# Kernel tuning notes

Measured on AMD Instinct MI355X. Metric: run time of the kernel, lower is better.

Reference implementation:

```python
import jax, jax.numpy as jnp
import numpy as np
from jax import lax

B, T = 64, 256
V, E, H, O = 50000, 256, 512, 50

def _xavier(key, shape):
    fan_in, fan_out = shape[1], shape[0]
    std = float(np.sqrt(2.0 / (fan_in + fan_out)))
    return jax.random.normal(key, shape, dtype=jnp.float32) * std

def lstm_scan(x, W_ih, W_hh, b, h0, c0):
    # x: (B, T, Din); precompute input projection for all timesteps
    xg = jnp.einsum('btd,gd->btg', x, W_ih) + b  # (B, T, 4H)
    def step(carry, xg_t):
        h, c = carry
        g = xg_t + h @ W_hh.T
        i, f, gg, o = jnp.split(g, 4, axis=-1)
        i = jax.nn.sigmoid(i); f = jax.nn.sigmoid(f)
        gg = jnp.tanh(gg); o = jax.nn.sigmoid(o)
        c = f * c + i * gg
        h = o * jnp.tanh(c)
        return (h, c), h
    _, hs = lax.scan(step, (h0, c0), jnp.transpose(xg, (1, 0, 2)))
    return jnp.transpose(hs, (1, 0, 2))  # (B, T, H)

def bilstm(x, W_ih, W_hh, b, h0, c0):
    # Faithful to source bugs: output_backward == output_forward flipped on BATCH dim
    out_f = lstm_scan(x, W_ih, W_hh, b, h0, c0)
    return jnp.concatenate([out_f, out_f[::-1]], axis=-1)  # (B, T, 2H)

def setup_inputs() -> dict:
    key = jax.random.key(0)
    ks = jax.random.split(key, 14)
    x = jax.random.randint(ks[0], (B, T), 0, V + 1, dtype=jnp.int32)
    emb = jax.random.normal(ks[1], (V + 1, E), dtype=jnp.float32)
    emb = emb.at[0].set(0.0)  # padding_idx=0
    s = 1.0 / np.sqrt(H)
    W_ih1 = jax.random.uniform(ks[2], (4 * H, E), minval=-s, maxval=s, dtype=jnp.float32)
    W_hh1 = jax.random.uniform(ks[3], (4 * H, H), minval=-s, maxval=s, dtype=jnp.float32)
    b1 = jax.random.uniform(ks[4], (4 * H,), minval=-s, maxval=s, dtype=jnp.float32)
    W_ih2 = jax.random.uniform(ks[5], (4 * H, 2 * H), minval=-s, maxval=s, dtype=jnp.float32)
    W_hh2 = jax.random.uniform(ks[6], (4 * H, H), minval=-s, maxval=s, dtype=jnp.float32)
    b2 = jax.random.uniform(ks[7], (4 * H,), minval=-s, maxval=s, dtype=jnp.float32)
    h01 = _xavier(ks[8], (B, H)); c01 = _xavier(ks[9], (B, H))
    h02 = _xavier(ks[10], (B, H)); c02 = _xavier(ks[11], (B, H))
    Wfc = jax.random.normal(ks[12], (O, 2 * H), dtype=jnp.float32) * 0.02
    bfc = jnp.zeros((O,), dtype=jnp.float32)
    return {"x": x, "emb": emb, "W_ih1": W_ih1, "W_hh1": W_hh1, "b1": b1,
            "h01": h01, "c01": c01, "W_ih2": W_ih2, "W_hh2": W_hh2, "b2": b2,
            "h02": h02, "c02": c02, "Wfc": Wfc, "bfc": bfc}

def reference(x, emb, W_ih1, W_hh1, b1, h01, c01, W_ih2, W_hh2, b2, h02, c02, Wfc, bfc):
    out = emb[x]                                   # (B, T, E) embedding lookup
    out = bilstm(out, W_ih1, W_hh1, b1, h01, c01)  # (B, T, 2H)
    out = bilstm(out, W_ih2, W_hh2, b2, h02, c02)  # (B, T, 2H)
    # dropout is identity at inference
    logits = jnp.einsum('btd,od->bto', out, Wfc) + bfc
    return jax.nn.log_softmax(logits, axis=-1)
```

## Files before the change

kernel.cpp:

```cpp
#include <hip/hip_runtime.h>


#define B_ 64
#define T_ 256
#define E_ 256
#define H_ 512
#define G_ 2048
#define O_ 50
#define NROW (B_ * T_)
#define RING 16

typedef unsigned short u16;
typedef unsigned int u32;
typedef unsigned long long u64;
typedef short bf16x8 __attribute__((ext_vector_type(8)));
typedef u16 u16x4 __attribute__((ext_vector_type(4)));
typedef u32 u32x4 __attribute__((ext_vector_type(4)));
typedef float f32x4 __attribute__((ext_vector_type(4)));

#define LD_AG(p)    __hip_atomic_load((p), __ATOMIC_RELAXED, __HIP_MEMORY_SCOPE_AGENT)
#define ST_AG(p, v) __hip_atomic_store((p), (v), __ATOMIC_RELAXED, __HIP_MEMORY_SCOPE_AGENT)

__device__ __forceinline__ u16 f2bf(float f) {
    unsigned u = __float_as_uint(f);
    return (u16)((u + 0x7fffu + ((u >> 16) & 1u)) >> 16);
}
__device__ __forceinline__ float bf2f(u16 x) {
    return __uint_as_float(((u32)x) << 16);
}
__device__ __forceinline__ float sigm(float x) {
    x = fminf(fmaxf(x, -30.f), 30.f);
    return 1.f / (1.f + __expf(-x));
}
__device__ __forceinline__ float tanh_f(float x) {
    x = fminf(fmaxf(x, -15.f), 15.f);
    float e = __expf(2.f * x);
    return (e - 1.f) / (e + 1.f);
}
__device__ __forceinline__ bf16x8 pack8(const float* p) {
    float4 v0 = *(const float4*)p;
    float4 v1 = *(const float4*)(p + 4);
    bf16x8 bb;
    bb[0] = (short)f2bf(v0.x); bb[1] = (short)f2bf(v0.y);
    bb[2] = (short)f2bf(v0.z); bb[3] = (short)f2bf(v0.w);
    bb[4] = (short)f2bf(v1.x); bb[5] = (short)f2bf(v1.y);
    bb[6] = (short)f2bf(v1.z); bb[7] = (short)f2bf(v1.w);
    return bb;
}

__global__ __launch_bounds__(256) void wfc_pad(
    const float* __restrict__ Wfc, u16* __restrict__ outp)
{
    int i = blockIdx.x * 256 + threadIdx.x;
    int row = i >> 8, c4 = (i & 255) * 4;
    u16x4 o = { 0, 0, 0, 0 };
    if (row < O_) {
        float4 v = *(const float4*)&Wfc[(size_t)row * 1024 + c4];
        o = u16x4{ f2bf(v.x), f2bf(v.y), f2bf(v.z), f2bf(v.w) };
    }
    *(u16x4*)&outp[(size_t)row * 1024 + c4] = o;
}

__global__ __launch_bounds__(256) void gemm_fused(
    const int* __restrict__ x, const float* __restrict__ emb,
    const float* __restrict__ Wih1, const float* __restrict__ b1,
    u16* __restrict__ C)
{
    __shared__ u16 Asm[128][40];
    __shared__ u16 Bsm[128][40];
    const int tid = threadIdx.x, lane = tid & 63, wave = tid >> 6;
    const int wr = wave >> 1, wc = wave & 1;
    const int bm = blockIdx.y, bn = blockIdx.x;
    f32x4 acc[4][4] = {};
    const int r = tid >> 1, kc = (tid & 1) * 16;
    const int grow = bm * 128 + r;
    const int xi = x[grow];
    const float* ag = emb  + (size_t)xi * E_;
    const float* bg = Wih1 + (size_t)(bn * 128 + r) * E_;
    for (int k0 = 0; k0 < E_; k0 += 32) {
        int col = k0 + kc;
        __syncthreads();
        *(bf16x8*)&Asm[r][kc]     = pack8(ag + col);
        *(bf16x8*)&Asm[r][kc + 8] = pack8(ag + col + 8);
        *(bf16x8*)&Bsm[r][kc]     = pack8(bg + col);
        *(bf16x8*)&Bsm[r][kc + 8] = pack8(bg + col + 8);
        __syncthreads();
        bf16x8 af[4], bf[4];
        #pragma unroll
        for (int mt = 0; mt < 4; mt++)
            af[mt] = *(const bf16x8*)&Asm[wr * 64 + mt * 16 + (lane & 15)][(lane >> 4) * 8];
        #pragma unroll
        for (int nt = 0; nt < 4; nt++)
            bf[nt] = *(const bf16x8*)&Bsm[wc * 64 + nt * 16 + (lane & 15)][(lane >> 4) * 8];
        #pragma unroll
        for (int mt = 0; mt < 4; mt++)
            #pragma unroll
            for (int nt = 0; nt < 4; nt++)
                acc[mt][nt] = __builtin_amdgcn_mfma_f32_16x16x32_bf16(
                    af[mt], bf[nt], acc[mt][nt], 0, 0, 0);
    }
    #pragma unroll
    for (int mt = 0; mt < 4; mt++) {
        #pragma unroll
        for (int nt = 0; nt < 4; nt++) {
            int col = bn * 128 + wc * 64 + nt * 16 + (lane & 15);
            float bv = b1[col];
            #pragma unroll
            for (int rr = 0; rr < 4; rr++) {
                int row = bm * 128 + wr * 64 + mt * 16 + (lane >> 4) * 4 + rr;
                C[(size_t)row * G_ + col] = f2bf(acc[mt][nt][rr] + bv);
            }
        }
    }
}

__global__ __launch_bounds__(512, 2) void scan12(
    const u16* __restrict__ xgb,
    const float* __restrict__ Whh1,
    const float* __restrict__ h01, const float* __restrict__ c01,
    u32* h1pub,
    u32* hx1,
    const float* __restrict__ Wih2,
    const float* __restrict__ Whh2,
    const float* __restrict__ b2,
    const float* __restrict__ h02, const float* __restrict__ c02,
    u32* ring,
    u32* hx2,
    u32* h2pk,
    int* sents)
{
    __shared__ u16 hl[16][520];
    __shared__ u16 a1cat[16][1032];
    __shared__ float glds[4][8][68];
    const int tid = threadIdx.x, lane = tid & 63, wave = tid >> 6;
    const int idx = blockIdx.x;
    const u64 tmask = 0xffff0000ffff0000ull;
    int budget = 1 << 20;

    if (idx < 64) {
        const int grp = idx & 7, ug = idx >> 3;
        const int gw = wave >> 1, uh = wave & 1;
        for (int j = tid; j < 8 * 260; j += 512) {
            int rw = 8 + j / 260, cl = (j % 260) * 2;
            *(u32*)&hl[rw][cl] = 0;
        }
        bf16x8 breg0[16], breg1[16];
        #pragma unroll
        for (int tt = 0; tt < 2; tt++) {
            const float* wr0 = Whh1
                + (size_t)(gw * H_ + ug * 64 + uh * 32 + tt * 16 + (lane & 15)) * H_
                + ((lane >> 4) * 8);
            #pragma unroll
            for (int kk = 0; kk < 16; kk++) {
                bf16x8 bb = pack8(wr0 + kk * 32);
                if (tt == 0) breg0[kk] = bb; else breg1[kk] = bb;
            }
        }
        const int bb_ = tid >> 6, uu = tid & 63;
        const int brow = grp * 8 + bb_, ucol = ug * 64 + uu;
        float c = c01[brow * H_ + ucol];
        #pragma unroll
        for (int j = 0; j < 8; ++j) {
            int k = tid + j * 512;
            int prow = k >> 9, pcol = k & 511;
            ST_AG(hx1 + (size_t)(grp * 8 + prow) * H_ + pcol,
                  (1u << 16) | (u32)f2bf(h01[(grp * 8 + prow) * H_ + pcol]));
        }
        const int crow = tid >> 6, ccol = (tid & 63) * 8;
        int* mysent = sents + grp * 32 + ug;
        __syncthreads();

        #pragma unroll 1
        for (int t = 0; t < T_; ++t) {
            const size_t xb = ((size_t)brow * T_ + t) * G_ + ucol;
            u16 xi = xgb[xb], xf = xgb[xb + 512];
            u16 xgg = xgb[xb + 1024], xo = xgb[xb + 1536];

            u64* src = (u64*)(hx1 + (size_t)(t & 1) * (B_ * H_)
                              + (size_t)(grp * 8 + crow) * H_ + ccol);
            const u32 wt = (u32)(t + 1);
            const u64 want = ((u64)wt << 16) | ((u64)wt << 48);
            u64 v0 = LD_AG(src + 0), v1 = LD_AG(src + 1);
            u64 v2 = LD_AG(src + 2), v3 = LD_AG(src + 3);
            int spin = 0;
            while ((((v0 ^ want) | (v1 ^ want) | (v2 ^ want) | (v3 ^ want)) & tmask) != 0) {
                if (--budget < 0) break;
                if (++spin > 2) __builtin_amdgcn_s_sleep(1);
                if ((v0 ^ want) & tmask) v0 = LD_AG(src + 0);
                if ((v1 ^ want) & tmask) v1 = LD_AG(src + 1);
                if ((v2 ^ want) & tmask) v2 = LD_AG(src + 2);
                if ((v3 ^ want) & tmask) v3 = LD_AG(src + 3);
            }
            u32x4 pk = { (u32)(v0 & 0xffff) | ((u32)(v0 >> 32) << 16),
                         (u32)(v1 & 0xffff) | ((u32)(v1 >> 32) << 16),
                         (u32)(v2 & 0xffff) | ((u32)(v2 >> 32) << 16),
                         (u32)(v3 & 0xffff) | ((u32)(v3 >> 32) << 16) };
            *(u32x4*)&hl[crow][ccol] = pk;
            __syncthreads();

            f32x4 a0 = {0,0,0,0}, a1 = {0,0,0,0}, a2 = {0,0,0,0}, a3 = {0,0,0,0};
            const int ar = lane & 15, ac = (lane >> 4) * 8;
            #pragma unroll
            for (int kk = 0; kk < 16; kk += 2) {
                bf16x8 f0 = *(const bf16x8*)&hl[ar][ac + kk * 32];
                bf16x8 f1 = *(const bf16x8*)&hl[ar][ac + (kk + 1) * 32];
                a0 = __builtin_amdgcn_mfma_f32_16x16x32_bf16(f0, breg0[kk],     a0, 0, 0, 0);
                a1 = __builtin_amdgcn_mfma_f32_16x16x32_bf16(f1, breg0[kk + 1], a1, 0, 0, 0);
                a2 = __builtin_amdgcn_mfma_f32_16x16x32_bf16(f0, breg1[kk],     a2, 0, 0, 0);
                a3 = __builtin_amdgcn_mfma_f32_16x16x32_bf16(f1, breg1[kk + 1], a3, 0, 0, 0);
            }
            #pragma unroll
            for (int rr = 0; rr < 4; rr++) {
                int br = (lane >> 4) * 4 + rr;
                if (br < 8) {
                    glds[gw][br][uh * 32 + (lane & 15)]      = a0[rr] + a1[rr];
                    glds[gw][br][uh * 32 + 16 + (lane & 15)] = a2[rr] + a3[rr];
                }
            }
            __syncthreads();

            float ip = glds[0][bb_][uu] + bf2f(xi);
            float fp = glds[1][bb_][uu] + bf2f(xf);
            float gp = glds[2][bb_][uu] + bf2f(xgg);
            float op = glds[3][bb_][uu] + bf2f(xo);
            float gi = sigm(ip), gf = sigm(fp), gc = tanh_f(gp), go = sigm(op);
            c = gf * c + gi * gc;
            float h = go * tanh_f(c);
            u32 me = f2bf(h);
            ST_AG(hx1 + (size_t)((t + 1) & 1) * (B_ * H_) + (size_t)brow * H_ + ucol,
                  ((u32)(t + 2) << 16) | me);
            u32 ot = (u32)__shfl_xor((int)me, 1);
            if (!(uu & 1))
                ST_AG(h1pub + ((size_t)brow * T_ + t) * 256 + (ucol >> 1),
                      me | (ot << 16));
            if (tid == 0) ST_AG(mysent, t + 1);
        }
        __syncthreads();
        if (tid == 0) ST_AG(mysent, T_ + 1);

    } else if (idx < 192) {
        const int bg = idx & 7, gg = (idx - 64) >> 3;
        for (int j = tid; j < 8 * 516; j += 512) {
            int rw = 8 + j / 516, cl = (j % 516) * 2;
            *(u32*)&a1cat[rw][cl] = 0;
        }
        const int gcol = gg * 128 + wave * 16 + (lane & 15);
        bf16x8 bi[32];
        {
            const float* wr0 = Wih2 + (size_t)gcol * 1024 + ((lane >> 4) * 8);
            #pragma unroll
            for (int kk = 0; kk < 32; kk++) bi[kk] = pack8(wr0 + kk * 32);
        }
        const float bias = b2[gcol];
        const int crow = tid >> 6, ccol = (tid & 63) * 16;
        const int myb  = bg * 8 + crow;
        const int myfb = (7 - bg) * 8 + (7 - crow);
        const u32* __restrict__ hbase =
            h1pub + (size_t)((ccol < 512) ? myb : myfb) * T_ * 256;
        const int  cadj  = (ccol < 512) ? (ccol >> 1) : ((ccol - 512) >> 1);
        __syncthreads();

        #pragma unroll 1
        for (int t = 0; t < T_; ++t) {
            if (tid < 16) {
                int g2 = (tid < 8) ? bg : (7 - bg);
                int* sp = sents + g2 * 32 + (tid & 7);
                const int want = t + 2;
                int spin = 0;
                while (LD_AG(sp) < want) {
                    if (--budget < 0) break;
                    if (++spin > 2) __builtin_amdgcn_s_sleep(2);
                }
            } else if (tid < 24 && t >= RING) {
                int* sp = sents + 512 + bg * 32 + (tid - 16);
                const int want = t - (RING - 1);
                int spin = 0;
                while (LD_AG(sp) < want) {
                    if (--budget < 0) break;
                    if (++spin > 2) __builtin_amdgcn_s_sleep(2);
                }
            }
            __syncthreads();

            const u32* s0 = hbase + (size_t)t * 256 + cadj;
            u32x4 q0 = *(const u32x4*)(s0);
            u32x4 q1 = *(const u32x4*)(s0 + 4);
            *(u32x4*)&a1cat[crow][ccol]     = q0;
            *(u32x4*)&a1cat[crow][ccol + 8] = q1;
            __syncthreads();

            f32x4 a0 = {0,0,0,0}, a1 = {0,0,0,0}, a2 = {0,0,0,0}, a3 = {0,0,0,0};
            const int ar = lane & 15, ac = (lane >> 4) * 8;
            #pragma unroll
            for (int kk = 0; kk < 32; kk += 4) {
                bf16x8 f0 = *(const bf16x8*)&a1cat[ar][ac + kk * 32];
                bf16x8 f1 = *(const bf16x8*)&a1cat[ar][ac + (kk + 1) * 32];
                bf16x8 f2 = *(const bf16x8*)&a1cat[ar][ac + (kk + 2) * 32];
                bf16x8 f3 = *(const bf16x8*)&a1cat[ar][ac + (kk + 3) * 32];
                a0 = __builtin_amdgcn_mfma_f32_16x16x32_bf16(f0, bi[kk],     a0, 0, 0, 0);
                a1 = __builtin_amdgcn_mfma_f32_16x16x32_bf16(f1, bi[kk + 1], a1, 0, 0, 0);
                a2 = __builtin_amdgcn_mfma_f32_16x16x32_bf16(f2, bi[kk + 2], a2, 0, 0, 0);
                a3 = __builtin_amdgcn_mfma_f32_16x16x32_bf16(f3, bi[kk + 3], a3, 0, 0, 0);
            }
            #pragma unroll
            for (int rr = 0; rr < 4; rr++) {
                int br = (lane >> 4) * 4 + rr;
                u32 me = f2bf((a0[rr] + a1[rr]) + (a2[rr] + a3[rr]) + bias);
                u32 ot = (u32)__shfl_xor((int)me, 1);
                if (br < 8 && !(lane & 1))
                    ST_AG(ring + ((size_t)(t & (RING - 1)) * B_ + bg * 8 + br) * 1024
                          + (gcol >> 1), me | (ot << 16));
            }
            __syncthreads();
            if (tid == 0) ST_AG(sents + 256 + bg * 32 + gg, t + 1);
        }

    } else {
        const int bg = idx & 7, ug = (idx - 192) >> 3;
        const int gw = wave >> 1, uh = wave & 1;
        for (int j = tid; j < 8 * 260; j += 512) {
            int rw = 8 + j / 260, cl = (j % 260) * 2;
            *(u32*)&hl[rw][cl] = 0;
        }
        bf16x8 breg0[16], breg1[16];
        #pragma unroll
        for (int tt = 0; tt < 2; tt++) {
            const float* wr0 = Whh2
                + (size_t)(gw * H_ + ug * 64 + uh * 32 + tt * 16 + (lane & 15)) * H_
                + ((lane >> 4) * 8);
            #pragma unroll
            for (int kk = 0; kk < 16; kk++) {
                bf16x8 bb = pack8(wr0 + kk * 32);
                if (tt == 0) breg0[kk] = bb; else breg1[kk] = bb;
            }
        }
        const int bb_ = tid >> 6, uu = tid & 63;
        const int brow = bg * 8 + bb_, ucol = ug * 64 + uu;
        float c = c02[brow * H_ + ucol];
        #pragma unroll
        for (int j = 0; j < 8; ++j) {
            int k = tid + j * 512;
            int prow = k >> 9, pcol = k & 511;
            ST_AG(hx2 + (size_t)(bg * 8 + prow) * H_ + pcol,
                  (1u << 16) | (u32)f2bf(h02[(bg * 8 + prow) * H_ + pcol]));
        }
        const int crow = tid >> 6, ccol = (tid & 63) * 8;
        __syncthreads();

        #pragma unroll 1
        for (int t = 0; t < T_; ++t) {
            if (tid < 16) {
                int* sp = sents + 256 + bg * 32 + tid;
                const int want = t + 1;
                int spin = 0;
                while (LD_AG(sp) < want) {
                    if (--budget < 0) break;
                    if (++spin > 2) __builtin_amdgcn_s_sleep(2);
                }
            }
            u64* src = (u64*)(hx2 + (size_t)(t & 1) * (B_ * H_)
                              + (size_t)(bg * 8 + crow) * H_ + ccol);
            const u32 wt = (u32)(t + 1);
            const u64 want = ((u64)wt << 16) | ((u64)wt << 48);
            u64 v0 = LD_AG(src + 0), v1 = LD_AG(src + 1);
            u64 v2 = LD_AG(src + 2), v3 = LD_AG(src + 3);
            int spin = 0;
            while ((((v0 ^ want) | (v1 ^ want) | (v2 ^ want) | (v3 ^ want)) & tmask) != 0) {
                if (--budget < 0) break;
                if (++spin > 2) __builtin_amdgcn_s_sleep(1);
                if ((v0 ^ want) & tmask) v0 = LD_AG(src + 0);
                if ((v1 ^ want) & tmask) v1 = LD_AG(src + 1);
                if ((v2 ^ want) & tmask) v2 = LD_AG(src + 2);
                if ((v3 ^ want) & tmask) v3 = LD_AG(src + 3);
            }
            u32x4 pk = { (u32)(v0 & 0xffff) | ((u32)(v0 >> 32) << 16),
                         (u32)(v1 & 0xffff) | ((u32)(v1 >> 32) << 16),
                         (u32)(v2 & 0xffff) | ((u32)(v2 >> 32) << 16),
                         (u32)(v3 & 0xffff) | ((u32)(v3 >> 32) << 16) };
            *(u32x4*)&hl[crow][ccol] = pk;
            __syncthreads();

            const size_t rb = ((size_t)(t & (RING - 1)) * B_ + brow) * 1024
                              + ug * 32 + (uu >> 1);
            u32 x0 = LD_AG(ring + rb);
            u32 x1 = LD_AG(ring + rb + 256);
            u32 x2 = LD_AG(ring + rb + 512);
            u32 x3 = LD_AG(ring + rb + 768);

            f32x4 a0 = {0,0,0,0}, a1 = {0,0,0,0}, a2 = {0,0,0,0}, a3 = {0,0,0,0};
            const int ar = lane & 15, ac = (lane >> 4) * 8;
            #pragma unroll
            for (int kk = 0; kk < 16; kk += 2) {
                bf16x8 f0 = *(const bf16x8*)&hl[ar][ac + kk * 32];
                bf16x8 f1 = *(const bf16x8*)&hl[ar][ac + (kk + 1) * 32];
                a0 = __builtin_amdgcn_mfma_f32_16x16x32_bf16(f0, breg0[kk],     a0, 0, 0, 0);
                a1 = __builtin_amdgcn_mfma_f32_16x16x32_bf16(f1, breg0[kk + 1], a1, 0, 0, 0);
                a2 = __builtin_amdgcn_mfma_f32_16x16x32_bf16(f0, breg1[kk],     a2, 0, 0, 0);
                a3 = __builtin_amdgcn_mfma_f32_16x16x32_bf16(f1, breg1[kk + 1], a3, 0, 0, 0);
            }
            #pragma unroll
            for (int rr = 0; rr < 4; rr++) {
                int br = (lane >> 4) * 4 + rr;
                if (br < 8) {
                    glds[gw][br][uh * 32 + (lane & 15)]      = a0[rr] + a1[rr];
                    glds[gw][br][uh * 32 + 16 + (lane & 15)] = a2[rr] + a3[rr];
                }
            }
            __syncthreads();
            if (tid == 0) ST_AG(sents + 512 + bg * 32 + ug, t + 1);

            const int sh = (uu & 1) * 16;
            float ip = glds[0][bb_][uu] + bf2f((u16)(x0 >> sh));
            float fp = glds[1][bb_][uu] + bf2f((u16)(x1 >> sh));
            float gp = glds[2][bb_][uu] + bf2f((u16)(x2 >> sh));
            float op = glds[3][bb_][uu] + bf2f((u16)(x3 >> sh));
            float gi = sigm(ip), gf = sigm(fp), gc = tanh_f(gp), go = sigm(op);
            c = gf * c + gi * gc;
            float h = go * tanh_f(c);
            u32 me = f2bf(h);
            ST_AG(hx2 + (size_t)((t + 1) & 1) * (B_ * H_) + (size_t)brow * H_ + ucol,
                  ((u32)(t + 2) << 16) | me);
            u32 ot = (u32)__shfl_xor((int)me, 1);
            if (!(uu & 1))
                h2pk[((size_t)brow * T_ + t) * 256 + (ucol >> 1)] = me | (ot << 16);
        }
    }
}

__global__ __launch_bounds__(256) void fc_mfma(
    const u16* __restrict__ h2, const u16* __restrict__ Wfcp,
    const float* __restrict__ bfc, float* __restrict__ out)
{
    __shared__ u16 hl[16][1032];
    __shared__ float cl[16][68];
    const int tid = threadIdx.x, lane = tid & 63, wave = tid >> 6;
    const int r0 = blockIdx.x * 16;
    const int b = r0 >> 8;
    const int fr0 = (63 - b) * T_ + (r0 & 255);
    #pragma unroll
    for (int j = 0; j < 16; ++j) {
        int k = tid + j * 256;
        int row = k >> 8, c4 = k & 255;
        const u16* src = (c4 < 128)
            ? h2 + (size_t)(r0 + row) * H_ + c4 * 4
            : h2 + (size_t)(fr0 + row) * H_ + (c4 - 128) * 4;
        *(u64*)&hl[row][c4 * 4] = *(const u64*)src;
    }
    __syncthreads();
    const int ar = lane & 15, ac = (lane >> 4) * 8;
    const u16* wrow = Wfcp + (size_t)(wave * 16 + ar) * 1024 + ac;
    f32x4 a0 = {0,0,0,0}, a1 = {0,0,0,0};
    #pragma unroll
    for (int kk = 0; kk < 32; kk += 2) {
        bf16x8 f0 = *(const bf16x8*)&hl[ar][ac + kk * 32];
        bf16x8 f1 = *(const bf16x8*)&hl[ar][ac + (kk + 1) * 32];
        bf16x8 w0 = *(const bf16x8*)(wrow + kk * 32);
        bf16x8 w1 = *(const bf16x8*)(wrow + (kk + 1) * 32);
        a0 = __builtin_amdgcn_mfma_f32_16x16x32_bf16(f0, w0, a0, 0, 0, 0);
        a1 = __builtin_amdgcn_mfma_f32_16x16x32_bf16(f1, w1, a1, 0, 0, 0);
    }
    #pragma unroll
    for (int rr = 0; rr < 4; rr++)
        cl[(lane >> 4) * 4 + rr][wave * 16 + ar] = a0[rr] + a1[rr];
    __syncthreads();
    #pragma unroll
    for (int rr2 = 0; rr2 < 4; rr2++) {
        int row = wave * 4 + rr2;
        float acc = (lane < O_) ? cl[row][lane] + bfc[lane] : -1e30f;
        float m = acc;
        #pragma unroll
        for (int off = 32; off > 0; off >>= 1) m = fmaxf(m, __shfl_xor(m, off));
        float e = (lane < O_) ? __expf(acc - m) : 0.f;
        float sm = e;
        #pragma unroll
        for (int off = 32; off > 0; off >>= 1) sm += __shfl_xor(sm, off);
        float lse = m + __logf(sm);
        if (lane < O_) out[(size_t)(r0 + row) * O_ + lane] = acc - lse;
    }
}


extern "C" void kernel_launch(void* const* d_in, const int* in_sizes, int n_in,
                              void* d_out, int out_size, void* d_ws, size_t ws_size,
                              hipStream_t stream)
{
    (void)in_sizes; (void)n_in; (void)out_size;
    const int*   x    = (const int*)  d_in[0];
    const float* emb  = (const float*)d_in[1];
    const float* Wih1 = (const float*)d_in[2];
    const float* Whh1 = (const float*)d_in[3];
    const float* b1   = (const float*)d_in[4];
    const float* h01  = (const float*)d_in[5];
    const float* c01  = (const float*)d_in[6];
    const float* Wih2 = (const float*)d_in[7];
    const float* Whh2 = (const float*)d_in[8];
    const float* b2   = (const float*)d_in[9];
    const float* h02  = (const float*)d_in[10];
    const float* c02  = (const float*)d_in[11];
    const float* Wfc  = (const float*)d_in[12];
    const float* bfc  = (const float*)d_in[13];
    float* out = (float*)d_out;

    char* ws = (char*)d_ws;
    size_t off = 0;
    auto alloc = [&](size_t bytes) {
        char* p = ws + off; off += (bytes + 255) & ~(size_t)255; return p;
    };
    u16* Wfcp  = (u16*)alloc((size_t)64 * 1024 * 2);
    u16* xgb   = (u16*)alloc((size_t)NROW * G_ * 2);
    u32* h1pub = (u32*)alloc((size_t)NROW * 256 * 4);
    u32* ring  = (u32*)alloc((size_t)RING * B_ * 1024 * 4);
    u32* hx1   = (u32*)alloc((size_t)2 * B_ * H_ * 4);
    u32* hx2   = (u32*)alloc((size_t)2 * B_ * H_ * 4);
    u32* h2pk  = (u32*)alloc((size_t)NROW * 256 * 4);
    int* sents = (int*)alloc(768 * sizeof(int));
    if (off > ws_size) return;

    hipMemsetAsync(sents, 0, 768 * sizeof(int), stream);
    wfc_pad<<<64, 256, 0, stream>>>(Wfc, Wfcp);

    gemm_fused<<<dim3(G_ / 128, NROW / 128), 256, 0, stream>>>(
        x, emb, Wih1, b1, xgb);

    scan12<<<256, 512, 0, stream>>>(xgb, Whh1, h01, c01, h1pub, hx1,
                                    Wih2, Whh2, b2, h02, c02, ring, hx2, h2pk,
                                    sents);

    fc_mfma<<<NROW / 16, 256, 0, stream>>>((const u16*)h2pk, Wfcp, bfc, out);
}
```

Before: 878.1 us.

## Compute LSTM gates in MFMA registers and double-buffer h tile to drop a barrier

Measured after the change: 1.481 ms. +68.6%, slower.

```diff
diff --git a/kernel.cpp b/kernel.cpp
--- a/kernel.cpp
+++ b/kernel.cpp
@@ -129,36 +129,41 @@
     u32* h2pk,
     int* sents)
 {
-    __shared__ u16 hl[16][520];
+    __shared__ u16 hl2[2][16][520];
     __shared__ u16 a1cat[16][1032];
-    __shared__ float glds[4][8][68];
     const int tid = threadIdx.x, lane = tid & 63, wave = tid >> 6;
     const int idx = blockIdx.x;
     const u64 tmask = 0xffff0000ffff0000ull;
     int budget = 1 << 20;
+    const int jj = lane & 15, kb = (lane >> 4) * 8;
 
     if (idx < 64) {
         const int grp = idx & 7, ug = idx >> 3;
-        const int gw = wave >> 1, uh = wave & 1;
-        for (int j = tid; j < 8 * 260; j += 512) {
-            int rw = 8 + j / 260, cl = (j % 260) * 2;
-            *(u32*)&hl[rw][cl] = 0;
-        }
+        for (int j = tid; j < 2 * 8 * 260; j += 512) {
+            int bu = j / (8 * 260), rem = j % (8 * 260);
+            int rw = 8 + rem / 260, cl = (rem % 260) * 2;
+            *(u32*)&hl2[bu][rw][cl] = 0;
+        }
+        const int gub = ug * 64 + (wave << 3);
         bf16x8 breg0[16], breg1[16];
-        #pragma unroll
-        for (int tt = 0; tt < 2; tt++) {
-            const float* wr0 = Whh1
-                + (size_t)(gw * H_ + ug * 64 + uh * 32 + tt * 16 + (lane & 15)) * H_
-                + ((lane >> 4) * 8);
+        {
+            const float* w0 = Whh1 + (size_t)((jj >> 3) * H_ + gub + (jj & 7)) * H_ + kb;
+            const float* w1 = Whh1 + (size_t)((2 + (jj >> 3)) * H_ + gub + (jj & 7)) * H_ + kb;
             #pragma unroll
             for (int kk = 0; kk < 16; kk++) {
-                bf16x8 bb = pack8(wr0 + kk * 32);
-                if (tt == 0) breg0[kk] = bb; else breg1[kk] = bb;
-            }
-        }
-        const int bb_ = tid >> 6, uu = tid & 63;
-        const int brow = grp * 8 + bb_, ucol = ug * 64 + uu;
-        float c = c01[brow * H_ + ucol];
+                breg0[kk] = pack8(w0 + kk * 32);
+                breg1[kk] = pack8(w1 + kk * 32);
+            }
+        }
+        const bool act = (jj < 8) && ((lane >> 4) < 2);
+        const int ucol = gub + jj;
+        int brow_[4];
+        float cst[4];
+        #pragma unroll
+        for (int rr = 0; rr < 4; rr++) {
+            brow_[rr] = grp * 8 + (lane >> 4) * 4 + rr;
+            cst[rr] = act ? c01[brow_[rr] * H_ + ucol] : 0.f;
+        }
         #pragma unroll
         for (int j = 0; j < 8; ++j) {
             int k = tid + j * 512;
@@ -172,10 +177,15 @@
 
         #pragma unroll 1
         for (int t = 0; t < T_; ++t) {
-            const size_t xb = ((size_t)brow * T_ + t) * G_ + ucol;
-            u16 xi = xgb[xb], xf = xgb[xb + 512];
-            u16 xgg = xgb[xb + 1024], xo = xgb[xb + 1536];
-
+            u16 xv[4][4] = {};
+            if (act) {
+                #pragma unroll
+                for (int rr = 0; rr < 4; rr++) {
+                    const size_t xb = ((size_t)brow_[rr] * T_ + t) * G_ + ucol;
+                    xv[rr][0] = xgb[xb];        xv[rr][1] = xgb[xb + 512];
+                    xv[rr][2] = xgb[xb + 1024]; xv[rr][3] = xgb[xb + 1536];
+                }
+            }
             u64* src = (u64*)(hx1 + (size_t)(t & 1) * (B_ * H_)
                               + (size_t)(grp * 8 + crow) * H_ + ccol);
             const u32 wt = (u32)(t + 1);
@@ -195,15 +205,14 @@
                          (u32)(v1 & 0xffff) | ((u32)(v1 >> 32) << 16),
                          (u32)(v2 & 0xffff) | ((u32)(v2 >> 32) << 16),
                          (u32)(v3 & 0xffff) | ((u32)(v3 >> 32) << 16) };
-            *(u32x4*)&hl[crow][ccol] = pk;
+            *(u32x4*)&hl2[t & 1][crow][ccol] = pk;
             __syncthreads();
 
             f32x4 a0 = {0,0,0,0}, a1 = {0,0,0,0}, a2 = {0,0,0,0}, a3 = {0,0,0,0};
-            const int ar = lane & 15, ac = (lane >> 4) * 8;
             #pragma unroll
             for (int kk = 0; kk < 16; kk += 2) {
-                bf16x8 f0 = *(const bf16x8*)&hl[ar][ac + kk * 32];
-                bf16x8 f1 = *(const bf16x8*)&hl[ar][ac + (kk + 1) * 32];
+                bf16x8 f0 = *(const bf16x8*)&hl2[t & 1][jj][kb + kk * 32];
+                bf16x8 f1 = *(const bf16x8*)&hl2[t & 1][jj][kb + (kk + 1) * 32];
                 a0 = __builtin_amdgcn_mfma_f32_16x16x32_bf16(f0, breg0[kk],     a0, 0, 0, 0);
                 a1 = __builtin_amdgcn_mfma_f32_16x16x32_bf16(f1, breg0[kk + 1], a1, 0, 0, 0);
                 a2 = __builtin_amdgcn_mfma_f32_16x16x32_bf16(f0, breg1[kk],     a2, 0, 0, 0);
@@ -211,28 +220,28 @@
             }
             #pragma unroll
             for (int rr = 0; rr < 4; rr++) {
-                int br = (lane >> 4) * 4 + rr;
-                if (br < 8) {
-                    glds[gw][br][uh * 32 + (lane & 15)]      = a0[rr] + a1[rr];
-                    glds[gw][br][uh * 32 + 16 + (lane & 15)] = a2[rr] + a3[rr];
-                }
-            }
-            __syncthreads();
-
-            float ip = glds[0][bb_][uu] + bf2f(xi);
-            float fp = glds[1][bb_][uu] + bf2f(xf);
-            float gp = glds[2][bb_][uu] + bf2f(xgg);
-            float op = glds[3][bb_][uu] + bf2f(xo);
-            float gi = sigm(ip), gf = sigm(fp), gc = tanh_f(gp), go = sigm(op);
-            c = gf * c + gi * gc;
-            float h = go * tanh_f(c);
-            u32 me = f2bf(h);
-            ST_AG(hx1 + (size_t)((t + 1) & 1) * (B_ * H_) + (size_t)brow * H_ + ucol,
-                  ((u32)(t + 2) << 16) | me);
-            u32 ot = (u32)__shfl_xor((int)me, 1);
-            if (!(uu & 1))
-                ST_AG(h1pub + ((size_t)brow * T_ + t) * 256 + (ucol >> 1),
-                      me | (ot << 16));
+                float ti = a0[rr] + a1[rr];
+                float tg = a2[rr] + a3[rr];
+                float fo = __shfl_xor(ti, 8);
+                float oo = __shfl_xor(tg, 8);
+                float ip = ti + bf2f(xv[rr][0]);
+                float fp = fo + bf2f(xv[rr][1]);
+                float gp = tg + bf2f(xv[rr][2]);
+                float op = oo + bf2f(xv[rr][3]);
+                float gi = sigm(ip), gf = sigm(fp), gc = tanh_f(gp), go = sigm(op);
+                cst[rr] = gf * cst[rr] + gi * gc;
+                float h = go * tanh_f(cst[rr]);
+                u32 me = f2bf(h);
+                u32 ot = (u32)__shfl_xor((int)me, 1);
+                if (act) {
+                    ST_AG(hx1 + (size_t)((t + 1) & 1) * (B_ * H_)
+                          + (size_t)brow_[rr] * H_ + ucol,
+                          ((u32)(t + 2) << 16) | me);
+                    if (!(jj & 1))
+                        ST_AG(h1pub + ((size_t)brow_[rr] * T_ + t) * 256 + (ucol >> 1),
+                              me | (ot << 16));
+                }
+            }
             if (tid == 0) ST_AG(mysent, t + 1);
         }
         __syncthreads();
@@ -317,26 +326,31 @@
 
     } else {
         const int bg = idx & 7, ug = (idx - 192) >> 3;
-        const int gw = wave >> 1, uh = wave & 1;
-        for (int j = tid; j < 8 * 260; j += 512) {
-            int rw = 8 + j / 260, cl = (j % 260) * 2;
-            *(u32*)&hl[rw][cl] = 0;
-        }
+        for (int j = tid; j < 2 * 8 * 260; j += 512) {
+            int bu = j / (8 * 260), rem = j % (8 * 260);
+            int rw = 8 + rem / 260, cl = (rem % 260) * 2;
+            *(u32*)&hl2[bu][rw][cl] = 0;
+        }
+        const int gub = ug * 64 + (wave << 3);
         bf16x8 breg0[16], breg1[16];
-        #pragma unroll
-        for (int tt = 0; tt < 2; tt++) {
-            const float* wr0 = Whh2
-                + (size_t)(gw * H_ + ug * 64 + uh * 32 + tt * 16 + (lane & 15)) * H_
-                + ((lane >> 4) * 8);
+        {
+            const float* w0 = Whh2 + (size_t)((jj >> 3) * H_ + gub + (jj & 7)) * H_ + kb;
+            const float* w1 = Whh2 + (size_t)((2 + (jj >> 3)) * H_ + gub + (jj & 7)) * H_ + kb;
             #pragma unroll
             for (int kk = 0; kk < 16; kk++) {
-                bf16x8 bb = pack8(wr0 + kk * 32);
-                if (tt == 0) breg0[kk] = bb; else breg1[kk] = bb;
-            }
-        }
-        const int bb_ = tid >> 6, uu = tid & 63;
-        const int brow = bg * 8 + bb_, ucol = ug * 64 + uu;
-        float c = c02[brow * H_ + ucol];
+                breg0[kk] = pack8(w0 + kk * 32);
+                breg1[kk] = pack8(w1 + kk * 32);
+            }
+        }
+        const bool act = (jj < 8) && ((lane >> 4) < 2);
+        const int ucol = gub + jj;
+        int brow_[4];
+        float cst[4];
+        #pragma unroll
+        for (int rr = 0; rr < 4; rr++) {
+            brow_[rr] = bg * 8 + (lane >> 4) * 4 + rr;
+            cst[rr] = act ? c02[brow_[rr] * H_ + ucol] : 0.f;
+        }
         #pragma unroll
         for (int j = 0; j < 8; ++j) {
             int k = tid + j * 512;
@@ -345,6 +359,7 @@
                   (1u << 16) | (u32)f2bf(h02[(bg * 8 + prow) * H_ + pcol]));
         }
         const int crow = tid >> 6, ccol = (tid & 63) * 8;
+        const int sh = (ucol & 1) * 16;
         __syncthreads();
 
         #pragma unroll 1
@@ -377,22 +392,29 @@
                          (u32)(v1 & 0xffff) | ((u32)(v1 >> 32) << 16),
                          (u32)(v2 & 0xffff) | ((u32)(v2 >> 32) << 16),
                          (u32)(v3 & 0xffff) | ((u32)(v3 >> 32) << 16) };
-            *(u32x4*)&hl[crow][ccol] = pk;
+            *(u32x4*)&hl2[t & 1][crow][ccol] = pk;
             __syncthreads();
 
-            const size_t rb = ((size_t)(t & (RING - 1)) * B_ + brow) * 1024
-                              + ug * 32 + (uu >> 1);
-            u32 x0 = LD_AG(ring + rb);
-            u32 x1 = LD_AG(ring + rb + 256);
-            u32 x2 = LD_AG(ring + rb + 512);
-            u32 x3 = LD_AG(ring + rb + 768);
+            if (tid == 0 && t > 0) ST_AG(sents + 512 + bg * 32 + ug, t);
+
+            u32 xw[4][4] = {};
+            if (act) {
+                const size_t sb = (size_t)(t & (RING - 1)) * (B_ * 1024);
+                #pragma unroll
+                for (int rr = 0; rr < 4; rr++) {
+                    const size_t rb = sb + (size_t)brow_[rr] * 1024 + (ucol >> 1);
+                    xw[rr][0] = LD_AG(ring + rb);
+                    xw[rr][1] = LD_AG(ring + rb + 256);
+                    xw[rr][2] = LD_AG(ring + rb + 512);
+                    xw[rr][3] = LD_AG(ring + rb + 768);
+                }
+            }
 
             f32x4 a0 = {0,0,0,0}, a1 = {0,0,0,0}, a2 = {0,0,0,0}, a3 = {0,0,0,0};
-            const int ar = lane & 15, ac = (lane >> 4) * 8;
             #pragma unroll
             for (int kk = 0; kk < 16; kk += 2) {
-                bf16x8 f0 = *(const bf16x8*)&hl[ar][ac + kk * 32];
-                bf16x8 f1 = *(const bf16x8*)&hl[ar][ac + (kk + 1) * 32];
+                bf16x8 f0 = *(const bf16x8*)&hl2[t & 1][jj][kb + kk * 32];
+                bf16x8 f1 = *(const bf16x8*)&hl2[t & 1][jj][kb + (kk + 1) * 32];
                 a0 = __builtin_amdgcn_mfma_f32_16x16x32_bf16(f0, breg0[kk],     a0, 0, 0, 0);
                 a1 = __builtin_amdgcn_mfma_f32_16x16x32_bf16(f1, breg0[kk + 1], a1, 0, 0, 0);
                 a2 = __builtin_amdgcn_mfma_f32_16x16x32_bf16(f0, breg1[kk],     a2, 0, 0, 0);
@@ -400,29 +422,28 @@
             }
             #pragma unroll
             for (int rr = 0; rr < 4; rr++) {
-                int br = (lane >> 4) * 4 + rr;
-                if (br < 8) {
-                    glds[gw][br][uh * 32 + (lane & 15)]      = a0[rr] + a1[rr];
-                    glds[gw][br][uh * 32 + 16 + (lane & 15)] = a2[rr] + a3[rr];
-                }
-            }
-            __syncthreads();
-            if (tid == 0) ST_AG(sents + 512 + bg * 32 + ug, t + 1);
-
-            const int sh = (uu & 1) * 16;
-            float ip = glds[0][bb_][uu] + bf2f((u16)(x0 >> sh));
-            float fp = glds[1][bb_][uu] + bf2f((u16)(x1 >> sh));
-            float gp = glds[2][bb_][uu] + bf2f((u16)(x2 >> sh));
-            float op = glds[3][bb_][uu] + bf2f((u16)(x3 >> sh));
-            float gi = sigm(ip), gf = sigm(fp), gc = tanh_f(gp), go = sigm(op);
-            c = gf * c + gi * gc;
-            float h = go * tanh_f(c);
-            u32 me = f2bf(h);
-            ST_AG(hx2 + (size_t)((t + 1) & 1) * (B_ * H_) + (size_t)brow * H_ + ucol,
-                  ((u32)(t + 2) << 16) | me);
-            u32 ot = (u32)__shfl_xor((int)me, 1);
-            if (!(uu & 1))
-                h2pk[((size_t)brow * T_ + t) * 256 + (ucol >> 1)] = me | (ot << 16);
+                float ti = a0[rr] + a1[rr];
+                float tg = a2[rr] + a3[rr];
+                float fo = __shfl_xor(ti, 8);
+                float oo = __shfl_xor(tg, 8);
+                float ip = ti + bf2f((u16)(xw[rr][0] >> sh));
+                float fp = fo + bf2f((u16)(xw[rr][1] >> sh));
+                float gp = tg + bf2f((u16)(xw[rr][2] >> sh));
+                float op = oo + bf2f((u16)(xw[rr][3] >> sh));
+                float gi = sigm(ip), gf = sigm(fp), gc = tanh_f(gp), go = sigm(op);
+                cst[rr] = gf * cst[rr] + gi * gc;
+                float h = go * tanh_f(cst[rr]);
+                u32 me = f2bf(h);
+                u32 ot = (u32)__shfl_xor((int)me, 1);
+                if (act) {
+                    ST_AG(hx2 + (size_t)((t + 1) & 1) * (B_ * H_)
+                          + (size_t)brow_[rr] * H_ + ucol,
+                          ((u32)(t + 2) << 16) | me);
+                    if (!(jj & 1))
+                        h2pk[((size_t)brow_[rr] * T_ + t) * 256 + (ucol >> 1)]
+                            = me | (ot << 16);
+                }
+            }
         }
     }
 }
```
